# Kernel tuning notes

Hardware: AMD Instinct MI355X
Metric: run time of the kernel (lower is better)

The kernel has to match this reference:

```python
import jax, jax.numpy as jnp
import numpy as np

REF_MIC_IDX = 0
LOAD = 0.001 / np.sqrt(2.0)  # diagonal loading added to BOTH real and imag parts in the torch code


def setup_inputs() -> dict:
    key = jax.random.key(0)
    k1, k2, k3 = jax.random.split(key, 3)
    shape = (8, 2, 8, 600, 257)  # N, RI, C, T, F
    return {
        "mixture": jax.random.normal(k1, shape, dtype=jnp.float32),
        "target": jax.random.normal(k2, shape, dtype=jnp.float32),
        "noise": jax.random.normal(k3, shape, dtype=jnp.float32),
    }


def _to_complex(x):
    # (N, 2, C, T, F) RI-stacked -> (N, C, T, F) complex
    return jax.lax.complex(x[:, 0], x[:, 1])


def reference(mixture, target, noise):
    N, _, C, T, F = mixture.shape
    y = _to_complex(mixture)  # (N, C, T, F)
    v = _to_complex(noise)
    cdtype = y.dtype

    # Time-averaged spatial covariance: sum_t V V^H / T -> (N, F, C, C)
    # (fused; the original materializes per-frame C x C matrices then sums)
    phi_v = jnp.einsum("nctf,ndtf->nfcd", v, jnp.conj(v)) / T
    phi_y = jnp.einsum("nctf,ndtf->nfcd", y, jnp.conj(y)) / T

    eye = jnp.eye(C, dtype=cdtype)
    # torch adds LOAD*eye to both real and imag slices -> complex (1+1j)*LOAD*eye
    phi_v = phi_v + (LOAD * (1.0 + 1.0j)) * eye

    G = jnp.linalg.inv(phi_v) @ phi_y  # (N, F, C, C)

    # l = trace(G) - C, where torch subtracts scalar C from both RI parts
    l = jnp.trace(G, axis1=-2, axis2=-1) - (C * (1.0 + 1.0j))  # (N, F)

    # H = (1/l) * (G - I) e_ref  -> column ref_mic_idx of (G - I)
    Ge = (G - eye)[..., :, REF_MIC_IDX]  # (N, F, C)
    H = Ge / l[..., None]  # (N, F, C)

    # Beamform: X(n,t,f) = sum_c conj(H)_{n,f,c} * y_{n,c,t,f}
    X = jnp.einsum("nfc,nctf->ntf", jnp.conj(H), y)  # (N, T, F)

    # Output in RI-stacked form with singleton channel: (N, 2, 1, T, F)
    est = jnp.stack([jnp.real(X), jnp.imag(X)], axis=1)[:, :, None]
    return est
```

## Files before the change

### kernel.cpp

```cpp
#include <hip/hip_runtime.h>


constexpr int N_  = 8;
constexpr int C_  = 8;
constexpr int T_  = 600;
constexpr int F_  = 257;
constexpr int TF_  = T_ * F_;
constexpr int CTF_ = C_ * TF_;
constexpr int NSTR_ = 2 * CTF_;
constexpr int NF_  = N_ * F_;
constexpr int NPAIR_ = 36;
constexpr float LOADC_ = 7.0710678118654755e-4f;
constexpr float INV_T_ = 1.0f / 600.0f;

#define SBAR() __builtin_amdgcn_sched_barrier(0)

struct cx { float r, i; };
__device__ __forceinline__ cx cmul(cx a, cx b) { return {a.r*b.r - a.i*b.i, a.r*b.i + a.i*b.r}; }
__device__ __forceinline__ cx csub(cx a, cx b) { return {a.r - b.r, a.i - b.i}; }
__device__ __forceinline__ cx cconj(cx a) { return {a.r, -a.i}; }
__device__ __forceinline__ cx cinv(cx a) {
    float id = 1.0f / (a.r*a.r + a.i*a.i);
    return {a.r*id, -a.i*id};
}
__device__ __forceinline__ cx cmadd(cx acc, cx a, cx b) {
    acc.r += a.r*b.r - a.i*b.i;
    acc.i += a.r*b.i + a.i*b.r;
    return acc;
}

template<int TSPLIT>
__global__ __launch_bounds__(64, 1) void cov_partial(
        const float* __restrict__ mix, const float* __restrict__ noi,
        float* __restrict__ part) {
    constexpr int TCHUNK = T_ / TSPLIT;
    constexpr int PIPE = 4;
    static_assert(TCHUNK > PIPE, "pipeline deeper than chunk");

    int f = blockIdx.x * 64 + threadIdx.x;
    if (f >= F_) return;
    int n = blockIdx.y;
    int z = blockIdx.z;
    int m = z & 1;
    int chunk = z >> 1;
    const float* src = m ? mix : noi;
    const float* pt = src + (size_t)n * NSTR_ + f + (size_t)(chunk * TCHUNK) * F_;

    float reB[PIPE][C_], imB[PIPE][C_];
#pragma unroll
    for (int s = 0; s < PIPE; ++s) {
        const float* pn = pt + (size_t)s * F_;
#pragma unroll
        for (int c = 0; c < C_; ++c) {
            reB[s][c] = pn[(size_t)c * TF_];
            imB[s][c] = pn[(size_t)c * TF_ + CTF_];
        }
    }
    SBAR();

    float accr[NPAIR_], acci[NPAIR_];
#pragma unroll
    for (int p = 0; p < NPAIR_; ++p) { accr[p] = 0.f; acci[p] = 0.f; }

#pragma unroll
    for (int tt = 0; tt < TCHUNK; ++tt) {
        const int s = tt % PIPE;
        const bool refill = (tt + PIPE < TCHUNK);

        float re[C_], im[C_];
#pragma unroll
        for (int c = 0; c < C_; ++c) { re[c] = reB[s][c]; im[c] = imB[s][c]; }

        if (refill) {
            const float* pn = pt + (size_t)(tt + PIPE) * F_;
#pragma unroll
            for (int c = 0; c < C_; ++c) {
                reB[s][c] = pn[(size_t)c * TF_];
                imB[s][c] = pn[(size_t)c * TF_ + CTF_];
            }
            SBAR();
        }

        int p = 0;
#pragma unroll
        for (int c = 0; c < C_; ++c) {
#pragma unroll
            for (int d = 0; d <= c; ++d, ++p) {
                accr[p] += re[c]*re[d] + im[c]*im[d];
                acci[p] += im[c]*re[d] - re[c]*im[d];
            }
        }
    }

    float* out = part + (size_t)((m * TSPLIT + chunk) * 72) * NF_ + n * F_ + f;
#pragma unroll
    for (int p = 0; p < NPAIR_; ++p) {
        out[(size_t)(2*p)   * NF_] = accr[p];
        out[(size_t)(2*p+1) * NF_] = acci[p];
    }
}

__global__ __launch_bounds__(256) void reduce_cov(float* __restrict__ part, int tsplit) {
    int flat = blockIdx.x * 256 + threadIdx.x;
    constexpr int NQ4 = NF_ / 4;
    if (flat >= 2 * 72 * NQ4) return;
    int idx4 = flat % NQ4;
    int z = flat / NQ4;
    int m = z / 72;
    int q = z % 72;
    const float4* p4 = (const float4*)(part) + ((size_t)((m * tsplit) * 72 + q) * NF_) / 4 + idx4;
    float4 s = {0.f, 0.f, 0.f, 0.f};
    for (int ch = 0; ch < tsplit; ++ch) {
        float4 v = p4[(size_t)(ch * 72) * NF_ / 4];
        s.x += v.x; s.y += v.y; s.z += v.z; s.w += v.w;
    }
    *(float4*)((float*)part + (size_t)((m * tsplit) * 72 + q) * NF_ + idx4 * 4) = s;
}

__global__ __launch_bounds__(64, 1) void solve_w(
        const float* __restrict__ part, float* __restrict__ W, size_t yBase) {
    int idx = blockIdx.x * 64 + threadIdx.x;
    if (idx >= NF_) return;

    const float* pv = part + idx;
    const float* py = part + yBase + idx;

    cx M[64];
#pragma unroll
    for (int c = 0; c < 8; ++c) {
#pragma unroll
        for (int d = 0; d <= c; ++d) {
            int p = c*(c+1)/2 + d;
            cx val = { pv[(size_t)(2*p) * NF_] * INV_T_,
                       pv[(size_t)(2*p+1) * NF_] * INV_T_ };
            if (d == c) { val.r += LOADC_; val.i += LOADC_; }
            M[c*8 + d] = val;
            if (d < c) M[d*8 + c] = cconj(val);
        }
    }

#pragma unroll
    for (int k = 0; k < 8; ++k) {
        cx p = cinv(M[k*8 + k]);
        M[k*8 + k] = p;
#pragma unroll
        for (int j = 0; j < 8; ++j) {
            if (j != k) M[k*8 + j] = cmul(M[k*8 + j], p);
        }
#pragma unroll
        for (int i = 0; i < 8; ++i) {
            if (i == k) continue;
            cx fkt = M[i*8 + k];
#pragma unroll
            for (int j = 0; j < 8; ++j) {
                if (j != k) M[i*8 + j] = csub(M[i*8 + j], cmul(fkt, M[k*8 + j]));
            }
            cx t = cmul(fkt, p);
            M[i*8 + k] = { -t.r, -t.i };
        }
    }

    cx tr = {0.f, 0.f};
    cx g0[8];
#pragma unroll
    for (int c = 0; c < 8; ++c) g0[c] = (cx){0.f, 0.f};

#pragma unroll
    for (int a = 0; a < 8; ++a) {
#pragma unroll
        for (int b = 0; b <= a; ++b) {
            int p = a*(a+1)/2 + b;
            cx yv = { py[(size_t)(2*p) * NF_] * INV_T_,
                      py[(size_t)(2*p+1) * NF_] * INV_T_ };
            tr = cmadd(tr, M[b*8 + a], yv);
            if (a != b) tr = cmadd(tr, M[a*8 + b], cconj(yv));
            if (b == 0) {
#pragma unroll
                for (int i = 0; i < 8; ++i) g0[i] = cmadd(g0[i], M[i*8 + a], yv);
            }
        }
    }

    cx l = { tr.r - 8.0f, tr.i - 8.0f };
    float iden = 1.0f / (l.r*l.r + l.i*l.i);

    float* w = W + (size_t)idx * 16;
#pragma unroll
    for (int c = 0; c < 8; ++c) {
        cx ge = g0[c];
        if (c == 0) ge.r -= 1.0f;
        w[2*c]     = (ge.r*l.r + ge.i*l.i) * iden;
        w[2*c + 1] = (ge.r*l.i - ge.i*l.r) * iden;
    }
}

__global__ __launch_bounds__(256) void beamform(
        const float* __restrict__ mix, const float* __restrict__ W,
        float* __restrict__ out) {
    int n = blockIdx.y;
    int j = blockIdx.x * 256 + threadIdx.x;
    if (j >= TF_) return;
    int f = j % F_;

    const float4* w4 = (const float4*)(W + (size_t)(n * F_ + f) * 16);
    float4 q0 = w4[0], q1 = w4[1], q2 = w4[2], q3 = w4[3];
    float wv[16] = { q0.x, q0.y, q0.z, q0.w,
                     q1.x, q1.y, q1.z, q1.w,
                     q2.x, q2.y, q2.z, q2.w,
                     q3.x, q3.y, q3.z, q3.w };

    const float* base = mix + (size_t)n * NSTR_ + j;
    float xr = 0.f, xi = 0.f;
#pragma unroll
    for (int c = 0; c < C_; ++c) {
        float yr = base[(size_t)c * TF_];
        float yi = base[(size_t)c * TF_ + CTF_];
        float wr = wv[2*c], wi = wv[2*c + 1];
        xr += wr*yr - wi*yi;
        xi += wr*yi + wi*yr;
    }
    float* op = out + (size_t)n * (2 * TF_);
    op[j]       = xr;
    op[TF_ + j] = xi;
}

extern "C" void kernel_launch(void* const* d_in, const int* in_sizes, int n_in,
                              void* d_out, int out_size, void* d_ws, size_t ws_size,
                              hipStream_t stream) {
    const float* mix = (const float*)d_in[0];
    const float* noi = (const float*)d_in[2];

    const size_t need25 = ((size_t)2 * 25 * 72 * NF_ + (size_t)16 * NF_) * 4;
    float* part = (float*)d_ws;
    int tsplit;
    if (ws_size >= need25) {
        tsplit = 25;
        cov_partial<25><<<dim3(5, N_, 2 * 25), 64, 0, stream>>>(mix, noi, part);
    } else {
        tsplit = 15;
        cov_partial<15><<<dim3(5, N_, 2 * 15), 64, 0, stream>>>(mix, noi, part);
    }
    float* W = part + (size_t)2 * tsplit * 72 * NF_;

    reduce_cov<<<dim3((2 * 72 * (NF_ / 4) + 255) / 256), 256, 0, stream>>>(part, tsplit);
    solve_w<<<dim3((NF_ + 63) / 64), 64, 0, stream>>>(part, W, (size_t)tsplit * 72 * NF_);
    beamform<<<dim3((TF_ + 255) / 256, N_), 256, 0, stream>>>(mix, W, (float*)d_out);
}
```

Measured before the change: 277.4 us.

## Stage covariance time slabs through LDS with vectorized loads; vectorize beamform

The covariance kernel now has one 320-thread block cover all frequencies for a time chunk. Each block cooperatively loads two-frame slabs into double-buffered shared memory with float2 global loads, then each thread accumulates its frequency from LDS. This replaces the old per-thread strided scalar loads with a register pipeline. The beamform kernel processes four consecutive elements per thread with float4 loads and stores, and the time split rises to 30 chunks. The costs are more syncthreads barriers, a 66KB LDS footprint per block that limits occupancy, and idle threads (tid>=257) during compute.

```diff
diff --git a/kernel.cpp b/kernel.cpp
--- a/kernel.cpp
+++ b/kernel.cpp
@@ -30,73 +30,100 @@
 }
 
 template<int TSPLIT>
-__global__ __launch_bounds__(64, 1) void cov_partial(
+__global__ __launch_bounds__(320, 3) void cov_partial(
         const float* __restrict__ mix, const float* __restrict__ noi,
         float* __restrict__ part) {
     constexpr int TCHUNK = T_ / TSPLIT;
-    constexpr int PIPE = 4;
-    static_assert(TCHUNK > PIPE, "pipeline deeper than chunk");
-
-    int f = blockIdx.x * 64 + threadIdx.x;
-    if (f >= F_) return;
-    int n = blockIdx.y;
-    int z = blockIdx.z;
-    int m = z & 1;
-    int chunk = z >> 1;
-    const float* src = m ? mix : noi;
-    const float* pt = src + (size_t)n * NSTR_ + f + (size_t)(chunk * TCHUNK) * F_;
-
-    float reB[PIPE][C_], imB[PIPE][C_];
-#pragma unroll
-    for (int s = 0; s < PIPE; ++s) {
-        const float* pn = pt + (size_t)s * F_;
-#pragma unroll
-        for (int c = 0; c < C_; ++c) {
-            reB[s][c] = pn[(size_t)c * TF_];
-            imB[s][c] = pn[(size_t)c * TF_ + CTF_];
-        }
-    }
+    static_assert(TCHUNK % 2 == 0, "TB=2 slabs need even TCHUNK");
+    constexpr int NS = TCHUNK / 2;
+    constexpr int NE = 16 * 257;
+    constexpr int KMAX = (NE + 319) / 320;
+
+    __shared__ float S[2][16][514];
+
+    const int tid = threadIdx.x;
+    const int chunk = blockIdx.x;
+    const int n = blockIdx.y;
+    const int m = blockIdx.z;
+    const float* src = (m ? mix : noi) + (size_t)n * NSTR_;
+    const int tBase = chunk * TCHUNK;
+
+    int gOff[KMAX], lOff[KMAX];
+#pragma unroll
+    for (int kk = 0; kk < KMAX; ++kk) {
+        int e = tid + 320 * kk;
+        if (e < NE) {
+            int pl = e / 257;
+            int off2 = (e - pl * 257) * 2;
+            int c = pl & 7;
+            gOff[kk] = ((pl < 8) ? c * TF_ : CTF_ + c * TF_) + off2;
+            lOff[kk] = pl * 514 + off2;
+        } else { gOff[kk] = 0; lOff[kk] = -1; }
+    }
+
+    float2 rg[KMAX];
+    auto stageRegs = [&](int t0) {
+        const int tF = t0 * F_;
+#pragma unroll
+        for (int kk = 0; kk < KMAX; ++kk)
+            if (lOff[kk] >= 0)
+                rg[kk] = *(const float2*)(src + (size_t)(gOff[kk] + tF));
+    };
+    auto writeLDS = [&](int buf) {
+        float* b = &S[buf][0][0];
+#pragma unroll
+        for (int kk = 0; kk < KMAX; ++kk)
+            if (lOff[kk] >= 0)
+                *(float2*)(b + lOff[kk]) = rg[kk];
+    };
+
+    float accr[NPAIR_], acci[NPAIR_];
+#pragma unroll
+    for (int p = 0; p < NPAIR_; ++p) { accr[p] = 0.f; acci[p] = 0.f; }
+
+    auto consume = [&](int buf) {
+        if (tid < F_) {
+#pragma unroll
+            for (int tt = 0; tt < 2; ++tt) {
+                float re[C_], im[C_];
+#pragma unroll
+                for (int c = 0; c < C_; ++c) {
+                    re[c] = S[buf][c][tt * 257 + tid];
+                    im[c] = S[buf][8 + c][tt * 257 + tid];
+                }
+                int p = 0;
+#pragma unroll
+                for (int c = 0; c < C_; ++c) {
+#pragma unroll
+                    for (int d = 0; d <= c; ++d, ++p) {
+                        accr[p] += re[c]*re[d] + im[c]*im[d];
+                        acci[p] += im[c]*re[d] - re[c]*im[d];
+                    }
+                }
+            }
+        }
+    };
+
+    stageRegs(tBase);
     SBAR();
-
-    float accr[NPAIR_], acci[NPAIR_];
-#pragma unroll
-    for (int p = 0; p < NPAIR_; ++p) { accr[p] = 0.f; acci[p] = 0.f; }
-
-#pragma unroll
-    for (int tt = 0; tt < TCHUNK; ++tt) {
-        const int s = tt % PIPE;
-        const bool refill = (tt + PIPE < TCHUNK);
-
-        float re[C_], im[C_];
-#pragma unroll
-        for (int c = 0; c < C_; ++c) { re[c] = reB[s][c]; im[c] = imB[s][c]; }
-
-        if (refill) {
-            const float* pn = pt + (size_t)(tt + PIPE) * F_;
-#pragma unroll
-            for (int c = 0; c < C_; ++c) {
-                reB[s][c] = pn[(size_t)c * TF_];
-                imB[s][c] = pn[(size_t)c * TF_ + CTF_];
-            }
-            SBAR();
-        }
-
-        int p = 0;
-#pragma unroll
-        for (int c = 0; c < C_; ++c) {
-#pragma unroll
-            for (int d = 0; d <= c; ++d, ++p) {
-                accr[p] += re[c]*re[d] + im[c]*im[d];
-                acci[p] += im[c]*re[d] - re[c]*im[d];
-            }
-        }
-    }
-
-    float* out = part + (size_t)((m * TSPLIT + chunk) * 72) * NF_ + n * F_ + f;
-#pragma unroll
-    for (int p = 0; p < NPAIR_; ++p) {
-        out[(size_t)(2*p)   * NF_] = accr[p];
-        out[(size_t)(2*p+1) * NF_] = acci[p];
+    writeLDS(0);
+    __syncthreads();
+
+    for (int k = 0; k < NS; ++k) {
+        const bool more = (k + 1 < NS);
+        if (more) { stageRegs(tBase + 2 * (k + 1)); SBAR(); }
+        consume(k & 1);
+        if (more) writeLDS((k + 1) & 1);
+        __syncthreads();
+    }
+
+    if (tid < F_) {
+        float* out = part + (size_t)((m * TSPLIT + chunk) * 72) * NF_ + n * F_ + tid;
+#pragma unroll
+        for (int p = 0; p < NPAIR_; ++p) {
+            out[(size_t)(2*p)   * NF_] = accr[p];
+            out[(size_t)(2*p+1) * NF_] = acci[p];
+        }
     }
 }
 
@@ -197,31 +224,40 @@
 __global__ __launch_bounds__(256) void beamform(
         const float* __restrict__ mix, const float* __restrict__ W,
         float* __restrict__ out) {
+    constexpr int U = TF_ / 4;
     int n = blockIdx.y;
-    int j = blockIdx.x * 256 + threadIdx.x;
-    if (j >= TF_) return;
-    int f = j % F_;
-
-    const float4* w4 = (const float4*)(W + (size_t)(n * F_ + f) * 16);
-    float4 q0 = w4[0], q1 = w4[1], q2 = w4[2], q3 = w4[3];
-    float wv[16] = { q0.x, q0.y, q0.z, q0.w,
-                     q1.x, q1.y, q1.z, q1.w,
-                     q2.x, q2.y, q2.z, q2.w,
-                     q3.x, q3.y, q3.z, q3.w };
-
-    const float* base = mix + (size_t)n * NSTR_ + j;
-    float xr = 0.f, xi = 0.f;
+    int u = blockIdx.x * 256 + threadIdx.x;
+    if (u >= U) return;
+    int j0 = 4 * u;
+    int f0 = j0 % F_;
+
+    float4 wv[4][4];
+#pragma unroll
+    for (int i = 0; i < 4; ++i) {
+        int fi = f0 + i; if (fi >= F_) fi -= F_;
+        const float4* wr = (const float4*)(W + (size_t)(n * F_ + fi) * 16);
+        wv[i][0] = wr[0]; wv[i][1] = wr[1]; wv[i][2] = wr[2]; wv[i][3] = wr[3];
+    }
+
+    const float* base = mix + (size_t)n * NSTR_ + j0;
+    float xr[4] = {0.f,0.f,0.f,0.f}, xi[4] = {0.f,0.f,0.f,0.f};
 #pragma unroll
     for (int c = 0; c < C_; ++c) {
-        float yr = base[(size_t)c * TF_];
-        float yi = base[(size_t)c * TF_ + CTF_];
-        float wr = wv[2*c], wi = wv[2*c + 1];
-        xr += wr*yr - wi*yi;
-        xi += wr*yi + wi*yr;
+        float4 yr4 = *(const float4*)(base + (size_t)c * TF_);
+        float4 yi4 = *(const float4*)(base + (size_t)c * TF_ + CTF_);
+        float yrA[4] = {yr4.x, yr4.y, yr4.z, yr4.w};
+        float yiA[4] = {yi4.x, yi4.y, yi4.z, yi4.w};
+#pragma unroll
+        for (int i = 0; i < 4; ++i) {
+            float wr_ = (c & 1) ? wv[i][c >> 1].z : wv[i][c >> 1].x;
+            float wi_ = (c & 1) ? wv[i][c >> 1].w : wv[i][c >> 1].y;
+            xr[i] += wr_*yrA[i] - wi_*yiA[i];
+            xi[i] += wr_*yiA[i] + wi_*yrA[i];
+        }
     }
     float* op = out + (size_t)n * (2 * TF_);
-    op[j]       = xr;
-    op[TF_ + j] = xi;
+    *(float4*)(op + j0)       = make_float4(xr[0], xr[1], xr[2], xr[3]);
+    *(float4*)(op + TF_ + j0) = make_float4(xi[0], xi[1], xi[2], xi[3]);
 }
 
 extern "C" void kernel_launch(void* const* d_in, const int* in_sizes, int n_in,
@@ -230,19 +266,19 @@
     const float* mix = (const float*)d_in[0];
     const float* noi = (const float*)d_in[2];
 
-    const size_t need25 = ((size_t)2 * 25 * 72 * NF_ + (size_t)16 * NF_) * 4;
+    const size_t need30 = ((size_t)2 * 30 * 72 * NF_ + (size_t)16 * NF_) * 4;
     float* part = (float*)d_ws;
     int tsplit;
-    if (ws_size >= need25) {
+    if (ws_size >= need30) {
+        tsplit = 30;
+        cov_partial<30><<<dim3(30, N_, 2), 320, 0, stream>>>(mix, noi, part);
+    } else {
         tsplit = 25;
-        cov_partial<25><<<dim3(5, N_, 2 * 25), 64, 0, stream>>>(mix, noi, part);
-    } else {
-        tsplit = 15;
-        cov_partial<15><<<dim3(5, N_, 2 * 15), 64, 0, stream>>>(mix, noi, part);
+        cov_partial<25><<<dim3(25, N_, 2), 320, 0, stream>>>(mix, noi, part);
     }
     float* W = part + (size_t)2 * tsplit * 72 * NF_;
 
     reduce_cov<<<dim3((2 * 72 * (NF_ / 4) + 255) / 256), 256, 0, stream>>>(part, tsplit);
     solve_w<<<dim3((NF_ + 63) / 64), 64, 0, stream>>>(part, W, (size_t)tsplit * 72 * NF_);
-    beamform<<<dim3((TF_ + 255) / 256, N_), 256, 0, stream>>>(mix, W, (float*)d_out);
-}
+    beamform<<<dim3((TF_ / 4 + 255) / 256, N_), 256, 0, stream>>>(mix, W, (float*)d_out);
+}
```

Result: slower. 354.6 us (+27.9%).
